# Kernel tuning notes

Measured on AMD Instinct MI355X. Metric: run time of the kernel, lower is better.

## Reference

```python
import jax, jax.numpy as jnp
import numpy as np

N_NODES = 89250


def _sage_conv(x, src, dst, w_l, w_r, b):
    # mean aggregation of neighbor messages x[src] at destination nodes
    msg = x[src]                                                # [E, C]
    agg = jax.ops.segment_sum(msg, dst, num_segments=N_NODES)   # [N, C]
    cnt = jax.ops.segment_sum(jnp.ones((src.shape[0],), x.dtype), dst,
                              num_segments=N_NODES)             # [N]
    mean = agg / jnp.clip(cnt, 1.0, None)[:, None]
    # PyG SAGEConv: lin_l(aggregated) + lin_r(x) + bias
    return mean @ w_l.T + x @ w_r.T + b


def setup_inputs() -> dict:
    key = jax.random.key(0)
    ks = jax.random.split(key, 9)
    N, E, F_IN = N_NODES, 899756, 500

    def glorot(k, shape):
        fan_in = shape[1]
        return jax.random.normal(k, shape, jnp.float32) / jnp.sqrt(jnp.float32(fan_in))

    x = jax.random.normal(ks[0], (N, F_IN), jnp.float32)
    edge_index = jax.random.randint(ks[1], (2, E), 0, N, jnp.int64 if jax.config.jax_enable_x64 else jnp.int32)
    return {
        "x": x,
        "edge_index": edge_index,
        "w_l1": glorot(ks[2], (512, F_IN)),
        "w_r1": glorot(ks[3], (512, F_IN)),
        "b1": jnp.zeros((512,), jnp.float32),
        "w_l2": glorot(ks[4], (256, 512)),
        "w_r2": glorot(ks[5], (256, 512)),
        "b2": jnp.zeros((256,), jnp.float32),
        "w_l3": glorot(ks[6], (7, 256)),
        "w_r3": glorot(ks[7], (7, 256)),
        "b3": jnp.zeros((7,), jnp.float32),
    }


def reference(x, edge_index, w_l1, w_r1, b1, w_l2, w_r2, b2, w_l3, w_r3, b3):
    src, dst = edge_index[0], edge_index[1]
    # eval mode: dropout is identity
    h = jax.nn.relu(_sage_conv(x, src, dst, w_l1, w_r1, b1))
    h = jax.nn.relu(_sage_conv(h, src, dst, w_l2, w_r2, b2))
    return _sage_conv(h, src, dst, w_l3, w_r3, b3)
```

## Files before the change

### kernel.cpp

```cpp
#include <hip/hip_runtime.h>
#include <cstdint>
#include <cstddef>

#define N_NODES 89250
#define M_PAD   89344
#define F0 500
#define F1 512
#define F2 256
#define F3 7
#define KP 512

typedef __attribute__((ext_vector_type(8))) short bf16x8;
typedef __attribute__((ext_vector_type(4))) float f32x4;

static inline int cdiv_i(int a, int b) { return (a + b - 1) / b; }

__device__ __forceinline__ unsigned short f2b(float f) {
  unsigned int u = __float_as_uint(f);
  u = (u + 0x7FFFu + ((u >> 16) & 1u)) >> 16;
  return (unsigned short)u;
}
__device__ __forceinline__ float b2f(unsigned short h) {
  return __uint_as_float(((unsigned int)h) << 16);
}

__global__ void degree_kernel(const int* __restrict__ dst, int* __restrict__ cnt, int E) {
  int stride = gridDim.x * blockDim.x;
  for (int i = blockIdx.x * blockDim.x + threadIdx.x; i < E; i += stride)
    atomicAdd(&cnt[dst[i]], 1);
}

__global__ __launch_bounds__(1024) void scan_partial(const int* __restrict__ cnt,
                                                     int* __restrict__ row_ptr,
                                                     int* __restrict__ bsum, int n) {
  __shared__ int sm[1024];
  const int i = blockIdx.x * 1024 + threadIdx.x;
  const int v = (i < n) ? cnt[i] : 0;
  sm[threadIdx.x] = v;
  __syncthreads();
  for (int off = 1; off < 1024; off <<= 1) {
    int t = (threadIdx.x >= off) ? sm[threadIdx.x - off] : 0;
    __syncthreads();
    sm[threadIdx.x] += t;
    __syncthreads();
  }
  if (i < n) row_ptr[i] = sm[threadIdx.x] - v;
  if (threadIdx.x == 1023) bsum[blockIdx.x] = sm[1023];
}

__global__ __launch_bounds__(1024) void scan_bsums(int* __restrict__ bsum, int nb) {
  __shared__ int sm[1024];
  const int v = (threadIdx.x < nb) ? bsum[threadIdx.x] : 0;
  sm[threadIdx.x] = v;
  __syncthreads();
  for (int off = 1; off < 1024; off <<= 1) {
    int t = (threadIdx.x >= off) ? sm[threadIdx.x - off] : 0;
    __syncthreads();
    sm[threadIdx.x] += t;
    __syncthreads();
  }
  if (threadIdx.x < nb) bsum[threadIdx.x] = sm[threadIdx.x] - v;
}

__global__ __launch_bounds__(1024) void scan_add(int* __restrict__ row_ptr,
                                                 const int* __restrict__ bsum,
                                                 int* __restrict__ cursor,
                                                 int n, int total) {
  const int i = blockIdx.x * 1024 + threadIdx.x;
  if (i < n) {
    const int v = row_ptr[i] + bsum[i >> 10];
    row_ptr[i] = v;
    cursor[i] = v;
  }
  if (i == 0) row_ptr[n] = total;
}

__global__ void fill_kernel(const int* __restrict__ src, const int* __restrict__ dst,
                            int* __restrict__ cursor, int* __restrict__ csr_src, int E) {
  int stride = gridDim.x * blockDim.x;
  for (int i = blockIdx.x * blockDim.x + threadIdx.x; i < E; i += stride) {
    const int p = atomicAdd(&cursor[dst[i]], 1);
    csr_src[p] = src[i];
  }
}

__global__ __launch_bounds__(256) void convert_x_kernel(const float* __restrict__ x,
                                                        unsigned short* __restrict__ xb) {
  const long long total = (long long)M_PAD * (KP / 8);
  const long long stride = (long long)gridDim.x * blockDim.x;
  for (long long idx = (long long)blockIdx.x * blockDim.x + threadIdx.x; idx < total; idx += stride) {
    const int node = (int)(idx >> 6);
    const int c8 = ((int)idx & 63) * 8;
    unsigned short r[8];
#pragma unroll
    for (int j = 0; j < 8; ++j) {
      const int c = c8 + j;
      float v = 0.0f;
      if (node < N_NODES && c < F0) v = x[(size_t)node * F0 + c];
      r[j] = f2b(v);
    }
    *reinterpret_cast<uint4*>(xb + (size_t)node * KP + c8) = *reinterpret_cast<const uint4*>(r);
  }
}

__global__ __launch_bounds__(256) void convert_w_all(
    const float* __restrict__ wl1, const float* __restrict__ wr1,
    const float* __restrict__ wl2, const float* __restrict__ wr2,
    const float* __restrict__ wl3, const float* __restrict__ wr3,
    unsigned short* __restrict__ wl1b, unsigned short* __restrict__ wr1b,
    unsigned short* __restrict__ w2b, unsigned short* __restrict__ w3b)
{
  int idx = blockIdx.x * 256 + threadIdx.x;
  const int S1 = F1 * KP;
  if (idx < S1) {
    const int j = idx >> 9, k = idx & 511;
    const bool in = (k < F0);
    wl1b[idx] = in ? f2b(wl1[(size_t)j * F0 + k]) : (unsigned short)0;
    wr1b[idx] = in ? f2b(wr1[(size_t)j * F0 + k]) : (unsigned short)0;
    return;
  }
  idx -= S1;
  const int S2 = F2 * KP;
  if (idx < S2) {
    w2b[idx] = f2b(wl2[idx]);
    w2b[S2 + idx] = f2b(wr2[idx]);
    return;
  }
  idx -= S2;
  if (idx < 16 * 256) {
    const int j = idx >> 8, k = idx & 255;
    float v = 0.0f;
    if (j < 7) v = wl3[(size_t)j * F2 + k];
    else if (j >= 8 && j < 15) v = wr3[(size_t)(j - 8) * F2 + k];
    w3b[idx] = f2b(v);
  }
}

__global__ __launch_bounds__(256) void gather_mean_bf512(
    const unsigned short* __restrict__ xb, const int* __restrict__ row_ptr,
    const int* __restrict__ csr_src, unsigned short* __restrict__ aggb)
{
  const int node = blockIdx.x * 4 + (threadIdx.x >> 6);
  const int t = threadIdx.x & 63;
  if (node >= M_PAD) return;
  if (node >= N_NODES) {
    *reinterpret_cast<uint4*>(aggb + (size_t)node * 512 + t * 8) = make_uint4(0, 0, 0, 0);
    return;
  }
  const int beg = row_ptr[node];
  const int end = row_ptr[node + 1];
  float acc[8] = {0.f, 0.f, 0.f, 0.f, 0.f, 0.f, 0.f, 0.f};
  for (int j = beg; j < end; j += 8) {
    uint4 v[8];
    float m[8];
#pragma unroll
    for (int u = 0; u < 8; ++u) {
      const int e = min(j + u, end - 1);
      m[u] = (j + u < end) ? 1.0f : 0.0f;
      v[u] = *reinterpret_cast<const uint4*>(xb + (size_t)csr_src[e] * 512 + t * 8);
    }
#pragma unroll
    for (int u = 0; u < 8; ++u) {
      const unsigned int w[4] = {v[u].x, v[u].y, v[u].z, v[u].w};
#pragma unroll
      for (int q = 0; q < 4; ++q) {
        acc[2 * q]     = fmaf(m[u], b2f((unsigned short)(w[q] & 0xFFFF)), acc[2 * q]);
        acc[2 * q + 1] = fmaf(m[u], b2f((unsigned short)(w[q] >> 16)),    acc[2 * q + 1]);
      }
    }
  }
  const int deg = end - beg;
  const float inv = 1.0f / (float)(deg > 1 ? deg : 1);
  unsigned short r[8];
#pragma unroll
  for (int q = 0; q < 8; ++q) r[q] = f2b(acc[q] * inv);
  *reinterpret_cast<uint4*>(aggb + (size_t)node * 512 + t * 8) = *reinterpret_cast<const uint4*>(r);
}

__global__ __launch_bounds__(256) void gemm_mfma(
    const unsigned short* __restrict__ A1, const unsigned short* __restrict__ A2,
    const unsigned short* __restrict__ B1, const unsigned short* __restrict__ B2,
    const float* __restrict__ bias, unsigned short* __restrict__ Cout,
    int J, int niter, int fuse, int relu)
{
  __shared__ __align__(16) unsigned short Alds[128 * 64];
  __shared__ __align__(16) unsigned short Blds[128 * 64];
  const int tid = threadIdx.x;
  const int lane = tid & 63;
  const int wid = tid >> 6;

  const int nwg = gridDim.x * gridDim.y;
  int wg = blockIdx.y * gridDim.x + blockIdx.x;
  const int cpx = nwg >> 3;
  wg = (wg & 7) * cpx + (wg >> 3);
  const int brow = (wg / gridDim.y) * 128;
  const int bcol = (wg % gridDim.y) * 128;

  const int wr = wid >> 1;
  const int wc = wid & 1;

  f32x4 acc[4][4];
#pragma unroll
  for (int m = 0; m < 4; ++m)
#pragma unroll
    for (int n = 0; n < 4; ++n) acc[m][n] = (f32x4){0.f, 0.f, 0.f, 0.f};

  const int srow = lane >> 3;
  const int gchunk = (lane & 7) ^ srow;
  const int fr = lane & 15;
  const int fk = lane >> 4;

  for (int it = 0; it < niter; ++it) {
    const unsigned short* __restrict__ A = (it < 8) ? A1 : A2;
    const unsigned short* __restrict__ B = (it < 8) ? B1 : B2;
    const int k0 = (it & 7) * 64;
    __syncthreads();
#pragma unroll
    for (int i = 0; i < 4; ++i) {
      const int r = i * 32 + wid * 8;
      __builtin_amdgcn_global_load_lds(
          (const __attribute__((address_space(1))) unsigned int*)(A + (size_t)(brow + r + srow) * KP + k0 + gchunk * 8),
          (__attribute__((address_space(3))) unsigned int*)(&Alds[r * 64]),
          16, 0, 0);
      __builtin_amdgcn_global_load_lds(
          (const __attribute__((address_space(1))) unsigned int*)(B + (size_t)(bcol + r + srow) * KP + k0 + gchunk * 8),
          (__attribute__((address_space(3))) unsigned int*)(&Blds[r * 64]),
          16, 0, 0);
    }
    __syncthreads();
#pragma unroll
    for (int ks = 0; ks < 2; ++ks) {
      bf16x8 a[4], b[4];
#pragma unroll
      for (int m = 0; m < 4; ++m) {
        const int row = wr * 64 + m * 16 + fr;
        a[m] = *reinterpret_cast<const bf16x8*>(&Alds[row * 64 + (((ks * 4 + fk) ^ (fr & 7)) * 8)]);
      }
#pragma unroll
      for (int n = 0; n < 4; ++n) {
        const int row = wc * 64 + n * 16 + fr;
        b[n] = *reinterpret_cast<const bf16x8*>(&Blds[row * 64 + (((ks * 4 + fk) ^ (fr & 7)) * 8)]);
      }
#pragma unroll
      for (int m = 0; m < 4; ++m)
#pragma unroll
        for (int n = 0; n < 4; ++n)
          acc[m][n] = __builtin_amdgcn_mfma_f32_16x16x32_bf16(a[m], b[n], acc[m][n], 0, 0, 0);
    }
  }

  const int crow0 = brow + wr * 64 + (lane >> 4) * 4;
  const int ccol0 = bcol + wc * 64 + (lane & 15);
#pragma unroll
  for (int n = 0; n < 4; ++n) {
    const int col = ccol0 + n * 16;
    const float bv = fuse ? bias[col] : 0.0f;
#pragma unroll
    for (int m = 0; m < 4; ++m) {
#pragma unroll
      for (int i = 0; i < 4; ++i) {
        const int row = crow0 + m * 16 + i;
        float v = acc[m][n][i] + bv;
        if (relu) v = fmaxf(v, 0.0f);
        Cout[(size_t)row * J + col] = f2b(v);
      }
    }
  }
}

__global__ __launch_bounds__(256) void combine2_kernel(
    const unsigned short* __restrict__ y, const int* __restrict__ row_ptr,
    const int* __restrict__ csr_src, const float* __restrict__ bias,
    unsigned short* __restrict__ h)
{
  const int node = blockIdx.x * 8 + (threadIdx.x >> 5);
  const int t = threadIdx.x & 31;
  if (node >= N_NODES) return;
  const int beg = row_ptr[node];
  const int end = row_ptr[node + 1];
  float acc[8] = {0.f, 0.f, 0.f, 0.f, 0.f, 0.f, 0.f, 0.f};
  for (int j = beg; j < end; j += 8) {
    uint4 v[8];
    float m[8];
#pragma unroll
    for (int u = 0; u < 8; ++u) {
      const int e = min(j + u, end - 1);
      m[u] = (j + u < end) ? 1.0f : 0.0f;
      v[u] = *reinterpret_cast<const uint4*>(y + (size_t)csr_src[e] * 512 + t * 8);
    }
#pragma unroll
    for (int u = 0; u < 8; ++u) {
      const unsigned int w[4] = {v[u].x, v[u].y, v[u].z, v[u].w};
#pragma unroll
      for (int q = 0; q < 4; ++q) {
        acc[2 * q]     = fmaf(m[u], b2f((unsigned short)(w[q] & 0xFFFF)), acc[2 * q]);
        acc[2 * q + 1] = fmaf(m[u], b2f((unsigned short)(w[q] >> 16)),    acc[2 * q + 1]);
      }
    }
  }
  const int deg = end - beg;
  const float inv = 1.0f / (float)(deg > 1 ? deg : 1);
  const uint4 rv = *reinterpret_cast<const uint4*>(y + (size_t)node * 512 + 256 + t * 8);
  const unsigned int ru[4] = {rv.x, rv.y, rv.z, rv.w};
  unsigned short r[8];
#pragma unroll
  for (int q = 0; q < 4; ++q) {
    const float y0 = b2f((unsigned short)(ru[q] & 0xFFFF));
    const float y1 = b2f((unsigned short)(ru[q] >> 16));
    const float c0 = acc[2 * q] * inv + y0 + bias[t * 8 + 2 * q];
    const float c1 = acc[2 * q + 1] * inv + y1 + bias[t * 8 + 2 * q + 1];
    r[2 * q]     = f2b(fmaxf(c0, 0.0f));
    r[2 * q + 1] = f2b(fmaxf(c1, 0.0f));
  }
  *reinterpret_cast<uint4*>(h + (size_t)node * 256 + t * 8) = *reinterpret_cast<const uint4*>(r);
}

__global__ __launch_bounds__(256) void gemm3_mfma(
    const unsigned short* __restrict__ h2b, const unsigned short* __restrict__ w3b,
    unsigned short* __restrict__ y3)
{
  const int wave = threadIdx.x >> 6, lane = threadIdx.x & 63;
  const int rowbase = blockIdx.x * 64 + wave * 16;
  const int fr = lane & 15, fk = lane >> 4;
  bf16x8 b[8];
#pragma unroll
  for (int ks = 0; ks < 8; ++ks)
    b[ks] = *reinterpret_cast<const bf16x8*>(w3b + fr * 256 + ks * 32 + fk * 8);
  f32x4 acc = (f32x4){0.f, 0.f, 0.f, 0.f};
#pragma unroll
  for (int ks = 0; ks < 8; ++ks) {
    const bf16x8 a = *reinterpret_cast<const bf16x8*>(h2b + (size_t)(rowbase + fr) * 256 + ks * 32 + fk * 8);
    acc = __builtin_amdgcn_mfma_f32_16x16x32_bf16(a, b[ks], acc, 0, 0, 0);
  }
  const int r0 = rowbase + fk * 4;
#pragma unroll
  for (int i = 0; i < 4; ++i)
    y3[(size_t)(r0 + i) * 16 + fr] = f2b(acc[i]);
}

__global__ __launch_bounds__(256) void combine3_kernel(
    const unsigned short* __restrict__ y3, const int* __restrict__ row_ptr,
    const int* __restrict__ csr_src, const float* __restrict__ b3,
    float* __restrict__ out, int N)
{
  const int node = blockIdx.x * 4 + (threadIdx.x >> 6);
  const int lane = threadIdx.x & 63;
  if (node >= N) return;
  const int beg = row_ptr[node];
  const int end = row_ptr[node + 1];
  float acc[7] = {0.f, 0.f, 0.f, 0.f, 0.f, 0.f, 0.f};
  for (int j = beg + lane; j < end; j += 64) {
    const int s = csr_src[j];
    const uint4 v = *reinterpret_cast<const uint4*>(y3 + (size_t)s * 16);
    const unsigned int u[4] = {v.x, v.y, v.z, v.w};
#pragma unroll
    for (int q = 0; q < 7; ++q) {
      const unsigned short hw = (unsigned short)((u[q >> 1] >> ((q & 1) * 16)) & 0xFFFF);
      acc[q] += b2f(hw);
    }
  }
#pragma unroll
  for (int q = 0; q < 7; ++q)
#pragma unroll
    for (int m = 1; m < 64; m <<= 1)
      acc[q] += __shfl_xor(acc[q], m, 64);
  if (lane == 0) {
    const int deg = end - beg;
    const float inv = 1.0f / (float)(deg > 1 ? deg : 1);
    const uint4 rv = *reinterpret_cast<const uint4*>(y3 + (size_t)node * 16 + 8);
    const unsigned int ru[4] = {rv.x, rv.y, rv.z, rv.w};
#pragma unroll
    for (int q = 0; q < 7; ++q) {
      const float self = b2f((unsigned short)((ru[q >> 1] >> ((q & 1) * 16)) & 0xFFFF));
      out[(size_t)node * F3 + q] = acc[q] * inv + self + b3[q];
    }
  }
}

extern "C" void kernel_launch(void* const* d_in, const int* in_sizes, int n_in,
                              void* d_out, int out_size, void* d_ws, size_t ws_size,
                              hipStream_t stream) {
  const float* x    = (const float*)d_in[0];
  const int*   ei   = (const int*)d_in[1];
  const float* w_l1 = (const float*)d_in[2];
  const float* w_r1 = (const float*)d_in[3];
  const float* b1   = (const float*)d_in[4];
  const float* w_l2 = (const float*)d_in[5];
  const float* w_r2 = (const float*)d_in[6];
  const float* b2   = (const float*)d_in[7];
  const float* w_l3 = (const float*)d_in[8];
  const float* w_r3 = (const float*)d_in[9];
  const float* b3   = (const float*)d_in[10];
  float* out = (float*)d_out;

  const int E = in_sizes[1] / 2;
  const int* src = ei;
  const int* dst = ei + E;

  char* p = (char*)d_ws;
  int* row_ptr = (int*)p;           p += (size_t)(N_NODES + 1) * 4;
  int* cnt     = (int*)p;           p += (size_t)N_NODES * 4;
  int* bsum    = (int*)p;           p += 1024 * 4;
  int* csr_src = (int*)p;           p += (size_t)E * 4;
  p = (char*)(((uintptr_t)p + 255) & ~(uintptr_t)255);
  unsigned short* xb   = (unsigned short*)p;  p += (size_t)M_PAD * KP * 2;
  unsigned short* aggb = (unsigned short*)p;  p += (size_t)M_PAD * KP * 2;
  unsigned short* h1b  = (unsigned short*)p;  p += (size_t)M_PAD * KP * 2;
  unsigned short* wl1b = (unsigned short*)p;  p += (size_t)F1 * KP * 2;
  unsigned short* wr1b = (unsigned short*)p;  p += (size_t)F1 * KP * 2;
  unsigned short* w2b  = (unsigned short*)p;  p += (size_t)F1 * KP * 2;
  unsigned short* w3b  = (unsigned short*)p;  p += (size_t)16 * F2 * 2;

  unsigned short* y2  = xb;
  unsigned short* h2b = aggb;
  unsigned short* y3  = h1b;

  const int nb = cdiv_i(N_NODES, 1024);

  hipMemsetAsync(cnt, 0, (size_t)N_NODES * sizeof(int), stream);
  degree_kernel<<<cdiv_i(E, 256), 256, 0, stream>>>(dst, cnt, E);
  scan_partial<<<nb, 1024, 0, stream>>>(cnt, row_ptr, bsum, N_NODES);
  scan_bsums<<<1, 1024, 0, stream>>>(bsum, nb);
  scan_add<<<nb, 1024, 0, stream>>>(row_ptr, bsum, cnt, N_NODES, E);
  fill_kernel<<<cdiv_i(E, 256), 256, 0, stream>>>(src, dst, cnt, csr_src, E);

  convert_x_kernel<<<2048, 256, 0, stream>>>(x, xb);
  {
    const int total = F1 * KP + F2 * KP + 16 * F2;
    convert_w_all<<<cdiv_i(total, 256), 256, 0, stream>>>(
        w_l1, w_r1, w_l2, w_r2, w_l3, w_r3, wl1b, wr1b, w2b, w3b);
  }

  gather_mean_bf512<<<cdiv_i(M_PAD, 4), 256, 0, stream>>>(xb, row_ptr, csr_src, aggb);
  {
    dim3 g(M_PAD / 128, F1 / 128);
    gemm_mfma<<<g, 256, 0, stream>>>(aggb, xb, wl1b, wr1b, b1, h1b, F1, 16, 1, 1);
  }

  {
    dim3 g(M_PAD / 128, 512 / 128);
    gemm_mfma<<<g, 256, 0, stream>>>(h1b, h1b, w2b, w2b, (const float*)nullptr, y2, 512, 8, 0, 0);
  }
  combine2_kernel<<<cdiv_i(N_NODES, 8), 256, 0, stream>>>(y2, row_ptr, csr_src, b2, h2b);

  gemm3_mfma<<<M_PAD / 64, 256, 0, stream>>>(h2b, w3b, y3);
  combine3_kernel<<<cdiv_i(N_NODES, 4), 256, 0, stream>>>(y3, row_ptr, csr_src, b3, out, N_NODES);
}
```

Baseline: 634.0 us.

## Use 256x256 double-buffered MFMA GEMM tiles with 8 waves and prefetch

Replaces the 128x128 single-buffered GEMM with a 256x256 tile kernel using 512 threads (8 waves, each computing 128x64) and two LDS buffers. The next K-stage is prefetched via global_load_lds while the current stage runs MFMAs, with manual s_waitcnt/s_barrier, s_setprio around MFMA bursts, and an XCD-aware workgroup remap. This targets exposed global-load latency and the global traffic per FLOP. In exchange it uses 128KB of LDS and more accumulator registers, which limits occupancy to one block per CU, and the grid shrinks to about 700 blocks.

```diff
diff --git a/kernel.cpp b/kernel.cpp
--- a/kernel.cpp
+++ b/kernel.cpp
@@ -177,86 +177,113 @@
   *reinterpret_cast<uint4*>(aggb + (size_t)node * 512 + t * 8) = *reinterpret_cast<const uint4*>(r);
 }
 
-__global__ __launch_bounds__(256) void gemm_mfma(
+__global__ __launch_bounds__(512) void gemm_mfma256(
     const unsigned short* __restrict__ A1, const unsigned short* __restrict__ A2,
     const unsigned short* __restrict__ B1, const unsigned short* __restrict__ B2,
     const float* __restrict__ bias, unsigned short* __restrict__ Cout,
-    int J, int niter, int fuse, int relu)
-{
-  __shared__ __align__(16) unsigned short Alds[128 * 64];
-  __shared__ __align__(16) unsigned short Blds[128 * 64];
+    int J, int nt, int fuse, int relu)
+{
+  __shared__ __align__(16) unsigned short Alds[2][256 * 64];
+  __shared__ __align__(16) unsigned short Blds[2][256 * 64];
   const int tid = threadIdx.x;
   const int lane = tid & 63;
-  const int wid = tid >> 6;
-
-  const int nwg = gridDim.x * gridDim.y;
-  int wg = blockIdx.y * gridDim.x + blockIdx.x;
-  const int cpx = nwg >> 3;
-  wg = (wg & 7) * cpx + (wg >> 3);
-  const int brow = (wg / gridDim.y) * 128;
-  const int bcol = (wg % gridDim.y) * 128;
-
-  const int wr = wid >> 1;
-  const int wc = wid & 1;
-
-  f32x4 acc[4][4];
-#pragma unroll
-  for (int m = 0; m < 4; ++m)
+  const int w = tid >> 6;
+  const int wm = w >> 2;
+  const int wn = w & 3;
+
+  int wg = blockIdx.x;
+  {
+    const int nwg = gridDim.x;
+    const int q = nwg >> 3, r = nwg & 7;
+    const int xcd = wg & 7, o = wg >> 3;
+    wg = (xcd < r ? xcd * (q + 1) : r * (q + 1) + (xcd - r) * q) + o;
+  }
+  const int ncol = J >> 8;
+  const int brow = (wg / ncol) * 256;
+  const int bcol = (wg % ncol) * 256;
+
+  f32x4 acc[8][4];
+#pragma unroll
+  for (int m = 0; m < 8; ++m)
 #pragma unroll
     for (int n = 0; n < 4; ++n) acc[m][n] = (f32x4){0.f, 0.f, 0.f, 0.f};
 
-  const int srow = lane >> 3;
-  const int gchunk = (lane & 7) ^ srow;
   const int fr = lane & 15;
   const int fk = lane >> 4;
-
-  for (int it = 0; it < niter; ++it) {
-    const unsigned short* __restrict__ A = (it < 8) ? A1 : A2;
-    const unsigned short* __restrict__ B = (it < 8) ? B1 : B2;
-    const int k0 = (it & 7) * 64;
-    __syncthreads();
+  const int srow_lo = lane >> 3;
+  const int schunk = (lane & 7) ^ (srow_lo & 7);
+
+  auto STAGE = [&](int t) {
+    const unsigned short* __restrict__ A = (t < 8) ? A1 : A2;
+    const unsigned short* __restrict__ B = (t < 8) ? B1 : B2;
+    const int k0 = (t & 7) * 64;
+    const int buf = t & 1;
 #pragma unroll
     for (int i = 0; i < 4; ++i) {
-      const int r = i * 32 + wid * 8;
+      const int rbase = i * 64 + w * 8;
+      const int row = rbase + srow_lo;
       __builtin_amdgcn_global_load_lds(
-          (const __attribute__((address_space(1))) unsigned int*)(A + (size_t)(brow + r + srow) * KP + k0 + gchunk * 8),
-          (__attribute__((address_space(3))) unsigned int*)(&Alds[r * 64]),
+          (const __attribute__((address_space(1))) unsigned int*)(A + (size_t)(brow + row) * KP + k0 + schunk * 8),
+          (__attribute__((address_space(3))) unsigned int*)(&Alds[buf][rbase * 64]),
           16, 0, 0);
       __builtin_amdgcn_global_load_lds(
-          (const __attribute__((address_space(1))) unsigned int*)(B + (size_t)(bcol + r + srow) * KP + k0 + gchunk * 8),
-          (__attribute__((address_space(3))) unsigned int*)(&Blds[r * 64]),
+          (const __attribute__((address_space(1))) unsigned int*)(B + (size_t)(bcol + row) * KP + k0 + schunk * 8),
+          (__attribute__((address_space(3))) unsigned int*)(&Blds[buf][rbase * 64]),
           16, 0, 0);
     }
-    __syncthreads();
-#pragma unroll
-    for (int ks = 0; ks < 2; ++ks) {
-      bf16x8 a[4], b[4];
+  };
+
+  STAGE(0);
+
+  for (int t = 0; t < nt; ++t) {
+    asm volatile("s_barrier" ::: "memory");
+    if (t + 1 < nt) {
+      STAGE(t + 1);
+      asm volatile("s_waitcnt vmcnt(8)" ::: "memory");
+    } else {
+      asm volatile("s_waitcnt vmcnt(0)" ::: "memory");
+    }
+    asm volatile("s_barrier" ::: "memory");
+
+    const int buf = t & 1;
+    bf16x8 bfr[2][4];
+#pragma unroll
+    for (int q = 0; q < 4; ++q) {
+      const int mh = q & 1;
+      const int ks = q >> 1;
+      bf16x8 a[4];
 #pragma unroll
       for (int m = 0; m < 4; ++m) {
-        const int row = wr * 64 + m * 16 + fr;
-        a[m] = *reinterpret_cast<const bf16x8*>(&Alds[row * 64 + (((ks * 4 + fk) ^ (fr & 7)) * 8)]);
+        const int row = wm * 128 + (mh * 4 + m) * 16 + fr;
+        const int ch = (ks * 4 + fk) ^ (row & 7);
+        a[m] = *reinterpret_cast<const bf16x8*>(&Alds[buf][row * 64 + ch * 8]);
       }
-#pragma unroll
-      for (int n = 0; n < 4; ++n) {
-        const int row = wc * 64 + n * 16 + fr;
-        b[n] = *reinterpret_cast<const bf16x8*>(&Blds[row * 64 + (((ks * 4 + fk) ^ (fr & 7)) * 8)]);
+      if (mh == 0) {
+#pragma unroll
+        for (int n = 0; n < 4; ++n) {
+          const int row = wn * 64 + n * 16 + fr;
+          const int ch = (ks * 4 + fk) ^ (row & 7);
+          bfr[ks][n] = *reinterpret_cast<const bf16x8*>(&Blds[buf][row * 64 + ch * 8]);
+        }
       }
+      __builtin_amdgcn_s_setprio(1);
 #pragma unroll
       for (int m = 0; m < 4; ++m)
 #pragma unroll
         for (int n = 0; n < 4; ++n)
-          acc[m][n] = __builtin_amdgcn_mfma_f32_16x16x32_bf16(a[m], b[n], acc[m][n], 0, 0, 0);
-    }
-  }
-
-  const int crow0 = brow + wr * 64 + (lane >> 4) * 4;
-  const int ccol0 = bcol + wc * 64 + (lane & 15);
+          acc[mh * 4 + m][n] = __builtin_amdgcn_mfma_f32_16x16x32_bf16(a[m], bfr[ks][n], acc[mh * 4 + m][n], 0, 0, 0);
+      __builtin_amdgcn_s_setprio(0);
+    }
+  }
+
+  const int crow0 = brow + wm * 128 + (lane >> 4) * 4;
+  const int ccol0 = bcol + wn * 64 + fr;
 #pragma unroll
   for (int n = 0; n < 4; ++n) {
     const int col = ccol0 + n * 16;
     const float bv = fuse ? bias[col] : 0.0f;
 #pragma unroll
-    for (int m = 0; m < 4; ++m) {
+    for (int m = 0; m < 8; ++m) {
 #pragma unroll
       for (int i = 0; i < 4; ++i) {
         const int row = crow0 + m * 16 + i;
@@ -432,15 +459,9 @@
   }
 
   gather_mean_bf512<<<cdiv_i(M_PAD, 4), 256, 0, stream>>>(xb, row_ptr, csr_src, aggb);
-  {
-    dim3 g(M_PAD / 128, F1 / 128);
-    gemm_mfma<<<g, 256, 0, stream>>>(aggb, xb, wl1b, wr1b, b1, h1b, F1, 16, 1, 1);
-  }
-
-  {
-    dim3 g(M_PAD / 128, 512 / 128);
-    gemm_mfma<<<g, 256, 0, stream>>>(h1b, h1b, w2b, w2b, (const float*)nullptr, y2, 512, 8, 0, 0);
-  }
+  gemm_mfma256<<<(M_PAD / 256) * 2, 512, 0, stream>>>(aggb, xb, wl1b, wr1b, b1, h1b, F1, 16, 1, 1);
+
+  gemm_mfma256<<<(M_PAD / 256) * 2, 512, 0, stream>>>(h1b, h1b, w2b, w2b, (const float*)nullptr, y2, 512, 8, 0, 0);
   combine2_kernel<<<cdiv_i(N_NODES, 8), 256, 0, stream>>>(y2, row_ptr, csr_src, b2, h2b);
 
   gemm3_mfma<<<M_PAD / 64, 256, 0, stream>>>(h2b, w3b, y3);
```

After: 677.2 us. 6.8% more time.

## Double-buffer LDS tiles in MFMA GEMM to overlap global loads with compute

Applied to the files above, without the earlier changes.

The GEMM now keeps two LDS buffers for the A and B tiles. It issues global-to-LDS loads for the next k-step before running the MFMAs on the current buffer, and replaces the pair of __syncthreads per iteration with a single waitcnt plus barrier. It also raises wave priority around the MFMA block. The goal is to hide global load latency behind matrix compute, at the cost of doubling LDS use to 64KB per block, which may reduce occupancy.

```diff
diff --git a/kernel.cpp b/kernel.cpp
--- a/kernel.cpp
+++ b/kernel.cpp
@@ -183,8 +183,8 @@
     const float* __restrict__ bias, unsigned short* __restrict__ Cout,
     int J, int niter, int fuse, int relu)
 {
-  __shared__ __align__(16) unsigned short Alds[128 * 64];
-  __shared__ __align__(16) unsigned short Blds[128 * 64];
+  __shared__ __align__(16) unsigned short Alds[2][128 * 64];
+  __shared__ __align__(16) unsigned short Blds[2][128 * 64];
   const int tid = threadIdx.x;
   const int lane = tid & 63;
   const int wid = tid >> 6;
@@ -206,47 +206,60 @@
     for (int n = 0; n < 4; ++n) acc[m][n] = (f32x4){0.f, 0.f, 0.f, 0.f};
 
   const int srow = lane >> 3;
-  const int gchunk = (lane & 7) ^ srow;
+  const int schunk = (lane & 7) ^ srow;
   const int fr = lane & 15;
   const int fk = lane >> 4;
 
-  for (int it = 0; it < niter; ++it) {
-    const unsigned short* __restrict__ A = (it < 8) ? A1 : A2;
-    const unsigned short* __restrict__ B = (it < 8) ? B1 : B2;
-    const int k0 = (it & 7) * 64;
-    __syncthreads();
+  auto STAGE = [&](int t) {
+    const unsigned short* __restrict__ A = (t < 8) ? A1 : A2;
+    const unsigned short* __restrict__ B = (t < 8) ? B1 : B2;
+    const int k0 = (t & 7) * 64;
+    const int buf = t & 1;
 #pragma unroll
     for (int i = 0; i < 4; ++i) {
-      const int r = i * 32 + wid * 8;
+      const int rbase = i * 32 + wid * 8;
+      const int row = rbase + srow;
       __builtin_amdgcn_global_load_lds(
-          (const __attribute__((address_space(1))) unsigned int*)(A + (size_t)(brow + r + srow) * KP + k0 + gchunk * 8),
-          (__attribute__((address_space(3))) unsigned int*)(&Alds[r * 64]),
+          (const __attribute__((address_space(1))) unsigned int*)(A + (size_t)(brow + row) * KP + k0 + schunk * 8),
+          (__attribute__((address_space(3))) unsigned int*)(&Alds[buf][rbase * 64]),
           16, 0, 0);
       __builtin_amdgcn_global_load_lds(
-          (const __attribute__((address_space(1))) unsigned int*)(B + (size_t)(bcol + r + srow) * KP + k0 + gchunk * 8),
-          (__attribute__((address_space(3))) unsigned int*)(&Blds[r * 64]),
+          (const __attribute__((address_space(1))) unsigned int*)(B + (size_t)(bcol + row) * KP + k0 + schunk * 8),
+          (__attribute__((address_space(3))) unsigned int*)(&Blds[buf][rbase * 64]),
           16, 0, 0);
     }
-    __syncthreads();
+  };
+
+  STAGE(0);
+  asm volatile("s_waitcnt vmcnt(0)" ::: "memory");
+  asm volatile("s_barrier" ::: "memory");
+
+  for (int t = 0; t < niter; ++t) {
+    if (t + 1 < niter) STAGE(t + 1);
+    const int buf = t & 1;
 #pragma unroll
     for (int ks = 0; ks < 2; ++ks) {
       bf16x8 a[4], b[4];
 #pragma unroll
       for (int m = 0; m < 4; ++m) {
         const int row = wr * 64 + m * 16 + fr;
-        a[m] = *reinterpret_cast<const bf16x8*>(&Alds[row * 64 + (((ks * 4 + fk) ^ (fr & 7)) * 8)]);
+        a[m] = *reinterpret_cast<const bf16x8*>(&Alds[buf][row * 64 + (((ks * 4 + fk) ^ (row & 7)) * 8)]);
       }
 #pragma unroll
       for (int n = 0; n < 4; ++n) {
         const int row = wc * 64 + n * 16 + fr;
-        b[n] = *reinterpret_cast<const bf16x8*>(&Blds[row * 64 + (((ks * 4 + fk) ^ (fr & 7)) * 8)]);
+        b[n] = *reinterpret_cast<const bf16x8*>(&Blds[buf][row * 64 + (((ks * 4 + fk) ^ (row & 7)) * 8)]);
       }
+      __builtin_amdgcn_s_setprio(1);
 #pragma unroll
       for (int m = 0; m < 4; ++m)
 #pragma unroll
         for (int n = 0; n < 4; ++n)
           acc[m][n] = __builtin_amdgcn_mfma_f32_16x16x32_bf16(a[m], b[n], acc[m][n], 0, 0, 0);
-    }
+      __builtin_amdgcn_s_setprio(0);
+    }
+    asm volatile("s_waitcnt vmcnt(0)" ::: "memory");
+    asm volatile("s_barrier" ::: "memory");
   }
 
   const int crow0 = brow + wr * 64 + (lane >> 4) * 4;
```

Result: slower. 652.1 us (+2.8%).
